# Optimization experiments

Hardware: AMD Instinct MI355X
Metric: run time of the kernel (lower is better)

Reference implementation:

```python
import jax, jax.numpy as jnp
import numpy as np

T, C, H = 8192, 2048, 8
D = C // H  # head_dim = 256
SCALE = D ** -0.5


def setup_inputs() -> dict:
    key = jax.random.key(0)
    ks = jax.random.split(key, 10)
    s = C ** -0.5  # Linear default init scale-ish
    return {
        "x": jax.random.normal(ks[0], (T, C), jnp.float32),
        "y": jax.random.normal(ks[1], (T, C), jnp.float32),
        "Wq": jax.random.normal(ks[2], (C, C), jnp.float32) * s,
        "bq": jax.random.normal(ks[3], (C,), jnp.float32) * s,
        "Wk": jax.random.normal(ks[4], (C, C), jnp.float32) * s,
        "bk": jax.random.normal(ks[5], (C,), jnp.float32) * s,
        "Wv": jax.random.normal(ks[6], (C, C), jnp.float32) * s,
        "bv": jax.random.normal(ks[7], (C,), jnp.float32) * s,
        "Wo": jax.random.normal(ks[8], (C, C), jnp.float32) * s,
        "bo": jax.random.normal(ks[9], (C,), jnp.float32) * s,
    }


def reference(x, y, Wq, bq, Wk, bk, Wv, bv, Wo, bo):
    # Linears (torch Linear: x @ W.T + b), then view [T, H, D]
    q = (x @ Wq.T + bq).reshape(T, H, D)
    k = (y @ Wk.T + bk).reshape(T, H, D)
    v = (y @ Wv.T + bv).reshape(T, H, D)
    # Faithful to source: T is the batch dim of the matmul, so attention is
    # a per-token [H, H] matrix across heads, NOT token-token attention.
    scores = jnp.einsum("thd,tgd->thg", q, k) * SCALE  # [T, H, H]
    attn = jax.nn.softmax(scores, axis=-1)
    out = jnp.einsum("thg,tgd->thd", attn, v).reshape(T, C)
    out = out @ Wo.T + bo
    return out + x
```

## Files before the change

### kernel.cpp

```cpp
#include <hip/hip_runtime.h>
#include <cstdint>
#include <cstddef>

#define T_TOK 8192
#define C_DIM 2048
#define H_HEADS 8
#define D_HEAD 256

typedef __bf16 v8bf __attribute__((ext_vector_type(8)));
typedef float v4f __attribute__((ext_vector_type(4)));
typedef float v8f __attribute__((ext_vector_type(8)));

__device__ __forceinline__ void async_load16(const void* gptr, void* lptr) {
    auto g = reinterpret_cast<__attribute__((address_space(1))) void*>(
        reinterpret_cast<uintptr_t>(gptr));
    auto l = reinterpret_cast<__attribute__((address_space(3))) void*>(
        static_cast<uint32_t>(reinterpret_cast<uintptr_t>(lptr)));
    __builtin_amdgcn_global_load_lds(g, l, 16, 0, 0);
}

__global__ __launch_bounds__(256) void cvt_kernel(
    const float* __restrict__ in, __bf16* __restrict__ out)
{
    const size_t i = ((size_t)blockIdx.x * 256 + threadIdx.x) * 8;
    v8f f = *(const v8f*)&in[i];
    v8bf b;
#pragma unroll
    for (int j = 0; j < 8; ++j) b[j] = (__bf16)f[j];
    *(v8bf*)&out[i] = b;
}

template <typename OutT>
__global__ __launch_bounds__(256) void gemm_bt_kernel(
    const __bf16* __restrict__ A, const __bf16* __restrict__ B,
    const float* __restrict__ bias, const float* __restrict__ residual,
    OutT* __restrict__ Cmat, int M, int N, int K)
{
    __shared__ __align__(16) __bf16 lds_a[128 * 64];
    __shared__ __align__(16) __bf16 lds_b[128 * 64];

    const int tid  = threadIdx.x;
    const int wave = tid >> 6;
    const int lane = tid & 63;

    const int nbm = M >> 7;
    const int per_xcd_m = nbm >> 3;
    const int b = blockIdx.x;
    const int xcd = b & 7;
    const int slot = b >> 3;
    const int m_blk = xcd * per_xcd_m + (slot % per_xcd_m);
    const int n_blk = slot / per_xcd_m;
    const int block_m = m_blk * 128;
    const int block_n = n_blk * 128;

    const int wm = (wave >> 1) * 64;
    const int wn = (wave & 1) * 64;
    const int lane_m = lane & 15;
    const int quad   = lane >> 4;

    v4f acc[4][4];
#pragma unroll
    for (int i = 0; i < 4; ++i)
#pragma unroll
        for (int j = 0; j < 4; ++j) {
            acc[i][j][0] = 0.f; acc[i][j][1] = 0.f;
            acc[i][j][2] = 0.f; acc[i][j][3] = 0.f;
        }

    for (int kt = 0; kt < K; kt += 64) {
        __syncthreads();
#pragma unroll
        for (int q = 0; q < 4; ++q) {
            const int li  = q * 256 + wave * 64 + lane;
            const int row = li >> 3;
            const int p   = li & 7;
            const int c   = (p - row) & 7;
            const int ldsbase = (q * 256 + wave * 64) * 8;
            async_load16(&A[(size_t)(block_m + row) * K + kt + c * 8], &lds_a[ldsbase]);
            async_load16(&B[(size_t)(block_n + row) * K + kt + c * 8], &lds_b[ldsbase]);
        }
        __syncthreads();

#pragma unroll
        for (int kk = 0; kk < 2; ++kk) {
            v8bf af[4], bfr[4];
#pragma unroll
            for (int i = 0; i < 4; ++i) {
                const int r = wm + i * 16 + lane_m;
                const int p = (kk * 4 + quad + r) & 7;
                af[i] = *(const v8bf*)&lds_a[r * 64 + p * 8];
            }
#pragma unroll
            for (int j = 0; j < 4; ++j) {
                const int r = wn + j * 16 + lane_m;
                const int p = (kk * 4 + quad + r) & 7;
                bfr[j] = *(const v8bf*)&lds_b[r * 64 + p * 8];
            }
#pragma unroll
            for (int i = 0; i < 4; ++i)
#pragma unroll
                for (int j = 0; j < 4; ++j)
                    acc[i][j] = __builtin_amdgcn_mfma_f32_16x16x32_bf16(
                        af[i], bfr[j], acc[i][j], 0, 0, 0);
        }
    }

#pragma unroll
    for (int i = 0; i < 4; ++i) {
        const int row0 = block_m + wm + i * 16 + quad * 4;
#pragma unroll
        for (int j = 0; j < 4; ++j) {
            const int col = block_n + wn + j * 16 + lane_m;
            const float bv = bias[col];
#pragma unroll
            for (int r = 0; r < 4; ++r) {
                float val = acc[i][j][r] + bv;
                const size_t off = (size_t)(row0 + r) * N + col;
                if (residual) val += residual[off];
                Cmat[off] = (OutT)val;
            }
        }
    }
}

__global__ __launch_bounds__(256) void attn_kernel(
    const __bf16* __restrict__ q, const __bf16* __restrict__ kv,
    __bf16* __restrict__ out)
{
    __shared__ __align__(16) __bf16 sq[4 * 2048];
    __shared__ __align__(16) __bf16 sk[4 * 2048];
    __shared__ __align__(16) __bf16 sv[4 * 2048];

    const int wave = threadIdx.x >> 6;
    const int lane = threadIdx.x & 63;
    const int t = blockIdx.x * 4 + wave;

    const __bf16* qt = q + (size_t)t * C_DIM;
    const __bf16* kt = kv + (size_t)t * 2 * C_DIM;
    const __bf16* vt = kt + C_DIM;
    __bf16* sqw = &sq[wave * C_DIM];
    __bf16* skw = &sk[wave * C_DIM];
    __bf16* svw = &sv[wave * C_DIM];

#pragma unroll
    for (int p = 0; p < 4; ++p) {
        const int idx = (p * 64 + lane) * 8;
        *(v8bf*)&sqw[idx] = *(const v8bf*)&qt[idx];
        *(v8bf*)&skw[idx] = *(const v8bf*)&kt[idx];
        *(v8bf*)&svw[idx] = *(const v8bf*)&vt[idx];
    }

    const int h = lane >> 3;
    const int g = lane & 7;
    float s = 0.f;
#pragma unroll 4
    for (int d = 0; d < D_HEAD; d += 8) {
        v8bf qa = *(const v8bf*)&sqw[h * D_HEAD + d];
        v8bf ka = *(const v8bf*)&skw[g * D_HEAD + d];
#pragma unroll
        for (int jj = 0; jj < 8; ++jj) s += (float)qa[jj] * (float)ka[jj];
    }
    s *= 0.0625f;

    float m = s;
    m = fmaxf(m, __shfl_xor(m, 1));
    m = fmaxf(m, __shfl_xor(m, 2));
    m = fmaxf(m, __shfl_xor(m, 4));
    const float e = __expf(s - m);
    float dsum = e;
    dsum += __shfl_xor(dsum, 1);
    dsum += __shfl_xor(dsum, 2);
    dsum += __shfl_xor(dsum, 4);
    const float p_attn = e / dsum;

    float attnv[8];
#pragma unroll
    for (int gg = 0; gg < 8; ++gg)
        attnv[gg] = __shfl(p_attn, (lane & 56) | gg);

    __bf16* outp = out + (size_t)t * C_DIM + h * D_HEAD + g * 32;
    const __bf16* vbase = &svw[g * 32];
#pragma unroll
    for (int dd = 0; dd < 32; dd += 8) {
        float o[8] = {0.f, 0.f, 0.f, 0.f, 0.f, 0.f, 0.f, 0.f};
#pragma unroll
        for (int gg = 0; gg < 8; ++gg) {
            v8bf vv = *(const v8bf*)&vbase[gg * D_HEAD + dd];
            const float pg = attnv[gg];
#pragma unroll
            for (int jj = 0; jj < 8; ++jj) o[jj] += pg * (float)vv[jj];
        }
        v8bf ov;
#pragma unroll
        for (int jj = 0; jj < 8; ++jj) ov[jj] = (__bf16)o[jj];
        *(v8bf*)&outp[dd] = ov;
    }
}

extern "C" void kernel_launch(void* const* d_in, const int* in_sizes, int n_in,
                              void* d_out, int out_size, void* d_ws, size_t ws_size,
                              hipStream_t stream) {
    const float* x  = (const float*)d_in[0];
    const float* y  = (const float*)d_in[1];
    const float* Wq = (const float*)d_in[2];
    const float* bq = (const float*)d_in[3];
    const float* Wk = (const float*)d_in[4];
    const float* bk = (const float*)d_in[5];
    const float* Wv = (const float*)d_in[6];
    const float* bv = (const float*)d_in[7];
    const float* Wo = (const float*)d_in[8];
    const float* bo = (const float*)d_in[9];
    float* out = (float*)d_out;

    const size_t TC = (size_t)T_TOK * C_DIM;
    const size_t CC = (size_t)C_DIM * C_DIM;

    __bf16* xb    = (__bf16*)d_ws;
    __bf16* kv_ws = xb;
    __bf16* yb    = xb + 2 * TC;
    __bf16* q_ws  = yb + TC;
    __bf16* Wb    = q_ws + TC;
    float*  bias_kv = (float*)(Wb + 2 * CC);
    __bf16* a_ws  = q_ws;

    dim3 gblock(256);
    const dim3 cvtTC(TC / (8 * 256)), cvtCC(CC / (8 * 256));

    cvt_kernel<<<cvtTC, gblock, 0, stream>>>(x, xb);
    cvt_kernel<<<cvtTC, gblock, 0, stream>>>(y, yb);
    hipMemcpyAsync(bias_kv,        bk, C_DIM * sizeof(float),
                   hipMemcpyDeviceToDevice, stream);
    hipMemcpyAsync(bias_kv + C_DIM, bv, C_DIM * sizeof(float),
                   hipMemcpyDeviceToDevice, stream);

    cvt_kernel<<<cvtCC, gblock, 0, stream>>>(Wq, Wb);
    gemm_bt_kernel<__bf16><<<dim3((T_TOK/128)*(C_DIM/128)), gblock, 0, stream>>>(
        xb, Wb, bq, nullptr, q_ws, T_TOK, C_DIM, C_DIM);

    cvt_kernel<<<cvtCC, gblock, 0, stream>>>(Wk, Wb);
    cvt_kernel<<<cvtCC, gblock, 0, stream>>>(Wv, Wb + CC);
    gemm_bt_kernel<__bf16><<<dim3((T_TOK/128)*(2*C_DIM/128)), gblock, 0, stream>>>(
        yb, Wb, bias_kv, nullptr, kv_ws, T_TOK, 2 * C_DIM, C_DIM);

    attn_kernel<<<dim3(T_TOK / 4), gblock, 0, stream>>>(q_ws, kv_ws, a_ws);

    cvt_kernel<<<cvtCC, gblock, 0, stream>>>(Wo, Wb);
    gemm_bt_kernel<float><<<dim3((T_TOK/128)*(C_DIM/128)), gblock, 0, stream>>>(
        a_ws, Wb, bo, x, out, T_TOK, C_DIM, C_DIM);
}
```

Baseline: 630.4 us.

## Rewrite GEMM as 256x256 tile with double-buffered async LDS pipeline

Replaces the 128x128 single-buffered GEMM with a 256x256 tile kernel using 512 threads, two LDS buffers, and prefetching two K-steps ahead so global loads overlap MFMA work. It also raises MFMA priority via s_setprio and remaps blocks to XCDs by N column groups. The larger tile increases reuse and cuts sync stalls, but uses 128KB LDS per block and more registers, which limits occupancy, and leaves fewer blocks per GEMM (256 or 512).

```diff
diff --git a/kernel.cpp b/kernel.cpp
--- a/kernel.cpp
+++ b/kernel.cpp
@@ -31,86 +31,120 @@
 }
 
 template <typename OutT>
-__global__ __launch_bounds__(256) void gemm_bt_kernel(
+__global__ __launch_bounds__(512, 2) void gemm256_kernel(
     const __bf16* __restrict__ A, const __bf16* __restrict__ B,
     const float* __restrict__ bias, const float* __restrict__ residual,
     OutT* __restrict__ Cmat, int M, int N, int K)
 {
-    __shared__ __align__(16) __bf16 lds_a[128 * 64];
-    __shared__ __align__(16) __bf16 lds_b[128 * 64];
+    __shared__ __align__(16) __bf16 lds_a[2][256 * 64];
+    __shared__ __align__(16) __bf16 lds_b[2][256 * 64];
 
     const int tid  = threadIdx.x;
     const int wave = tid >> 6;
     const int lane = tid & 63;
-
-    const int nbm = M >> 7;
-    const int per_xcd_m = nbm >> 3;
-    const int b = blockIdx.x;
-    const int xcd = b & 7;
-    const int slot = b >> 3;
-    const int m_blk = xcd * per_xcd_m + (slot % per_xcd_m);
-    const int n_blk = slot / per_xcd_m;
-    const int block_m = m_blk * 128;
-    const int block_n = n_blk * 128;
-
-    const int wm = (wave >> 1) * 64;
-    const int wn = (wave & 1) * 64;
     const int lane_m = lane & 15;
     const int quad   = lane >> 4;
 
-    v4f acc[4][4];
-#pragma unroll
-    for (int i = 0; i < 4; ++i)
+    const int nbm = M >> 8;
+    const int nbn = N >> 8;
+    const int npx = nbn >> 3;
+    const int bb   = blockIdx.x;
+    const int xcd  = bb & 7;
+    const int slot = bb >> 3;
+    const int n_blk = xcd * npx + slot / nbm;
+    const int m_blk = slot % nbm;
+    const int block_m = m_blk << 8;
+    const int block_n = n_blk << 8;
+
+    const int wave_m = wave >> 2;
+    const int wave_n = wave & 3;
+
+    const __bf16* aSrc[4];
+    const __bf16* bSrc[4];
+    int ldsOff[4];
+#pragma unroll
+    for (int r = 0; r < 4; ++r) {
+        const int li  = r * 512 + tid;
+        const int row = li >> 3;
+        const int p   = li & 7;
+        const int c   = (p - row) & 7;
+        aSrc[r] = &A[(size_t)(block_m + row) * K + c * 8];
+        bSrc[r] = &B[(size_t)(block_n + row) * K + c * 8];
+        ldsOff[r] = (r * 512 + wave * 64) * 8;
+    }
+
+    auto stage = [&](int buf, int kt) {
+#pragma unroll
+        for (int r = 0; r < 4; ++r) {
+            async_load16(aSrc[r] + kt, &lds_a[buf][ldsOff[r]]);
+            async_load16(bSrc[r] + kt, &lds_b[buf][ldsOff[r]]);
+        }
+    };
+
+    v4f acc[8][4];
+#pragma unroll
+    for (int i = 0; i < 8; ++i)
 #pragma unroll
         for (int j = 0; j < 4; ++j) {
             acc[i][j][0] = 0.f; acc[i][j][1] = 0.f;
             acc[i][j][2] = 0.f; acc[i][j][3] = 0.f;
         }
 
-    for (int kt = 0; kt < K; kt += 64) {
-        __syncthreads();
-#pragma unroll
-        for (int q = 0; q < 4; ++q) {
-            const int li  = q * 256 + wave * 64 + lane;
-            const int row = li >> 3;
-            const int p   = li & 7;
-            const int c   = (p - row) & 7;
-            const int ldsbase = (q * 256 + wave * 64) * 8;
-            async_load16(&A[(size_t)(block_m + row) * K + kt + c * 8], &lds_a[ldsbase]);
-            async_load16(&B[(size_t)(block_n + row) * K + kt + c * 8], &lds_b[ldsbase]);
-        }
-        __syncthreads();
-
+    stage(0, 0);
+    stage(1, 64);
+    asm volatile("s_waitcnt vmcnt(8)" ::: "memory");
+    __builtin_amdgcn_s_barrier();
+
+    const int NT = K >> 6;
+    int cur = 0;
+    for (int t = 0; t < NT; ++t) {
+        const int kt2 = (t + 2) << 6;
 #pragma unroll
         for (int kk = 0; kk < 2; ++kk) {
-            v8bf af[4], bfr[4];
-#pragma unroll
-            for (int i = 0; i < 4; ++i) {
-                const int r = wm + i * 16 + lane_m;
+            v8bf af[8], bfr[4];
+#pragma unroll
+            for (int i = 0; i < 8; ++i) {
+                const int r = wave_m * 128 + i * 16 + lane_m;
                 const int p = (kk * 4 + quad + r) & 7;
-                af[i] = *(const v8bf*)&lds_a[r * 64 + p * 8];
+                af[i] = *(const v8bf*)&lds_a[cur][r * 64 + p * 8];
             }
 #pragma unroll
             for (int j = 0; j < 4; ++j) {
-                const int r = wn + j * 16 + lane_m;
+                const int r = wave_n * 64 + j * 16 + lane_m;
                 const int p = (kk * 4 + quad + r) & 7;
-                bfr[j] = *(const v8bf*)&lds_b[r * 64 + p * 8];
-            }
-#pragma unroll
-            for (int i = 0; i < 4; ++i)
+                bfr[j] = *(const v8bf*)&lds_b[cur][r * 64 + p * 8];
+            }
+            if (kk == 1) {
+                asm volatile("s_waitcnt lgkmcnt(0)" ::: "memory");
+                __builtin_amdgcn_s_barrier();
+                if (t + 2 < NT) stage(cur, kt2);
+            }
+            __builtin_amdgcn_s_setprio(1);
+#pragma unroll
+            for (int i = 0; i < 8; ++i)
 #pragma unroll
                 for (int j = 0; j < 4; ++j)
                     acc[i][j] = __builtin_amdgcn_mfma_f32_16x16x32_bf16(
                         af[i], bfr[j], acc[i][j], 0, 0, 0);
-        }
-    }
-
-#pragma unroll
-    for (int i = 0; i < 4; ++i) {
-        const int row0 = block_m + wm + i * 16 + quad * 4;
+            __builtin_amdgcn_s_setprio(0);
+        }
+        if (t < NT - 1) {
+            if (t + 2 < NT) {
+                asm volatile("s_waitcnt vmcnt(8)" ::: "memory");
+            } else {
+                asm volatile("s_waitcnt vmcnt(0)" ::: "memory");
+            }
+            __builtin_amdgcn_s_barrier();
+        }
+        cur ^= 1;
+    }
+
+#pragma unroll
+    for (int i = 0; i < 8; ++i) {
+        const int row0 = block_m + wave_m * 128 + i * 16 + quad * 4;
 #pragma unroll
         for (int j = 0; j < 4; ++j) {
-            const int col = block_n + wn + j * 16 + lane_m;
+            const int col = block_n + wave_n * 64 + j * 16 + lane_m;
             const float bv = bias[col];
 #pragma unroll
             for (int r = 0; r < 4; ++r) {
@@ -223,28 +257,28 @@
     float*  bias_kv = (float*)(Wb + 2 * CC);
     __bf16* a_ws  = q_ws;
 
-    dim3 gblock(256);
+    dim3 cblock(256), gblock(512);
     const dim3 cvtTC(TC / (8 * 256)), cvtCC(CC / (8 * 256));
 
-    cvt_kernel<<<cvtTC, gblock, 0, stream>>>(x, xb);
-    cvt_kernel<<<cvtTC, gblock, 0, stream>>>(y, yb);
+    cvt_kernel<<<cvtTC, cblock, 0, stream>>>(x, xb);
+    cvt_kernel<<<cvtTC, cblock, 0, stream>>>(y, yb);
     hipMemcpyAsync(bias_kv,        bk, C_DIM * sizeof(float),
                    hipMemcpyDeviceToDevice, stream);
     hipMemcpyAsync(bias_kv + C_DIM, bv, C_DIM * sizeof(float),
                    hipMemcpyDeviceToDevice, stream);
 
-    cvt_kernel<<<cvtCC, gblock, 0, stream>>>(Wq, Wb);
-    gemm_bt_kernel<__bf16><<<dim3((T_TOK/128)*(C_DIM/128)), gblock, 0, stream>>>(
+    cvt_kernel<<<cvtCC, cblock, 0, stream>>>(Wq, Wb);
+    gemm256_kernel<__bf16><<<dim3((T_TOK/256)*(C_DIM/256)), gblock, 0, stream>>>(
         xb, Wb, bq, nullptr, q_ws, T_TOK, C_DIM, C_DIM);
 
-    cvt_kernel<<<cvtCC, gblock, 0, stream>>>(Wk, Wb);
-    cvt_kernel<<<cvtCC, gblock, 0, stream>>>(Wv, Wb + CC);
-    gemm_bt_kernel<__bf16><<<dim3((T_TOK/128)*(2*C_DIM/128)), gblock, 0, stream>>>(
+    cvt_kernel<<<cvtCC, cblock, 0, stream>>>(Wk, Wb);
+    cvt_kernel<<<cvtCC, cblock, 0, stream>>>(Wv, Wb + CC);
+    gemm256_kernel<__bf16><<<dim3((T_TOK/256)*(2*C_DIM/256)), gblock, 0, stream>>>(
         yb, Wb, bias_kv, nullptr, kv_ws, T_TOK, 2 * C_DIM, C_DIM);
 
-    attn_kernel<<<dim3(T_TOK / 4), gblock, 0, stream>>>(q_ws, kv_ws, a_ws);
-
-    cvt_kernel<<<cvtCC, gblock, 0, stream>>>(Wo, Wb);
-    gemm_bt_kernel<float><<<dim3((T_TOK/128)*(C_DIM/128)), gblock, 0, stream>>>(
+    attn_kernel<<<dim3(T_TOK / 4), cblock, 0, stream>>>(q_ws, kv_ws, a_ws);
+
+    cvt_kernel<<<cvtCC, cblock, 0, stream>>>(Wo, Wb);
+    gemm256_kernel<float><<<dim3((T_TOK/256)*(C_DIM/256)), gblock, 0, stream>>>(
         a_ws, Wb, bo, x, out, T_TOK, C_DIM, C_DIM);
 }
```

Result: faster. 569.4 us (-9.7%).
